# Optimization experiments

Hardware: AMD Instinct MI355X
Metric: run time of the kernel (lower is better)

Reference implementation:

```python
import jax, jax.numpy as jnp
import numpy as np

B = 2048
V = 50257
T = 64
D = 32
N_IN = 128
N_OUT = 128
N_HID = 1500
N_LAYERS = 5
N_BIAS = 2
K = 45  # int(edge_prob * n_nodes) fixed in-degree per receiving node
HID_PER_LAYER = N_HID // N_LAYERS  # 300
N_RECV = N_HID + N_OUT  # 1628 receiving nodes (hidden + output)


def _build_graph(rng):
    """Topological random wiring: each receiving node picks K predecessors
    among all earlier nodes (inputs, bias, earlier hidden layers)."""
    src_rows = []
    avail = N_IN + N_BIAS  # nodes available before first hidden layer
    for _ in range(N_LAYERS):
        src_rows.append(rng.integers(0, avail, size=(HID_PER_LAYER, K)))
        avail += HID_PER_LAYER
    src_rows.append(rng.integers(0, avail, size=(N_OUT, K)))  # output nodes
    return np.concatenate(src_rows, axis=0).astype(np.int32)  # [N_RECV, K]


def setup_inputs() -> dict:
    key = jax.random.key(0)
    ks = jax.random.split(key, 6)
    rng = np.random.default_rng(0)
    ids = jax.random.randint(ks[0], (B, T), 0, V, dtype=jnp.int32)
    token_emb = jax.random.normal(ks[1], (V, D), dtype=jnp.float32) * 0.02
    in_w = jax.random.normal(ks[2], (N_IN, T * D), dtype=jnp.float32) / np.sqrt(T * D)
    in_b = jnp.zeros((N_IN,), dtype=jnp.float32)
    src_idx = jnp.asarray(_build_graph(rng))  # [N_RECV, K] int32
    rwnn_w = jax.random.normal(ks[3], (N_RECV, K), dtype=jnp.float32) / np.sqrt(K)
    out_w = jax.random.normal(ks[4], (V, N_OUT), dtype=jnp.float32) / np.sqrt(N_OUT)
    out_b = jnp.zeros((V,), dtype=jnp.float32)
    return {"ids": ids, "token_emb": token_emb, "in_w": in_w, "in_b": in_b,
            "src_idx": src_idx, "rwnn_w": rwnn_w, "out_w": out_w, "out_b": out_b}


def _rwnn_forward(x, src_idx, rwnn_w):
    """x: [B, N_IN] -> [B, N_OUT]. Sparse random-wired DAG forward."""
    b = x.shape[0]
    vals = jnp.concatenate([x, jnp.ones((b, N_BIAS), dtype=x.dtype)], axis=1)
    off = 0
    for _ in range(N_LAYERS):
        s = src_idx[off:off + HID_PER_LAYER]          # [300, K]
        w = rwnn_w[off:off + HID_PER_LAYER]           # [300, K]
        gathered = vals[:, s]                          # [B, 300, K] irregular gather
        new = jnp.tanh(jnp.einsum('bnk,nk->bn', gathered, w))
        vals = jnp.concatenate([vals, new], axis=1)
        off += HID_PER_LAYER
    s = src_idx[off:off + N_OUT]
    w = rwnn_w[off:off + N_OUT]
    return jnp.tanh(jnp.einsum('bnk,nk->bn', vals[:, s], w))  # [B, N_OUT]


def reference(ids, token_emb, in_w, in_b, src_idx, rwnn_w, out_w, out_b):
    emb = token_emb[ids]                     # [B, T, D]
    flat = emb.reshape(emb.shape[0], T * D)  # [B, T*D]
    x = flat @ in_w.T + in_b                 # [B, N_IN]
    h = _rwnn_forward(x, src_idx, rwnn_w)    # [B, N_OUT]
    logits = h @ out_w.T + out_b             # [B, V]
    return logits
```

## Files before the change

kernel.cpp:

```cpp
#include <hip/hip_runtime.h>

#define B_SZ   2048
#define V_SZ   50257
#define TD     2048
#define NIN    128
#define NOUT   128
#define NRECV  1628
#define KDEG   45
#define KPAD   48
#define HPL    300
#define VALSN  1632

typedef __bf16 bf16x8 __attribute__((ext_vector_type(8)));
typedef float  floatx16 __attribute__((ext_vector_type(16)));

__device__ __forceinline__ unsigned short f2bf(float f) {
  unsigned u = __float_as_uint(f);
  u += 0x7fffu + ((u >> 16) & 1u);
  return (unsigned short)(u >> 16);
}

__device__ __forceinline__ float tanh_fast(float v) {
  float e = __builtin_amdgcn_exp2f(v * 2.88539008177793f);
  return 1.0f - 2.0f * __builtin_amdgcn_rcpf(1.0f + e);
}

__device__ __forceinline__ bf16x8 cvt8(float4 lo, float4 hi) {
  bf16x8 d;
  d[0] = (__bf16)lo.x; d[1] = (__bf16)lo.y; d[2] = (__bf16)lo.z; d[3] = (__bf16)lo.w;
  d[4] = (__bf16)hi.x; d[5] = (__bf16)hi.y; d[6] = (__bf16)hi.z; d[7] = (__bf16)hi.w;
  return d;
}

#define P1 1608224
#define P2 65536
#define P4 78144
#define PREP_TOTAL (P1 + P2 + P4)
#define PREP_BLOCKS ((PREP_TOTAL + 255) / 256)

__global__ __launch_bounds__(256) void prep_kernel(
    const float* __restrict__ in_w,
    const int* __restrict__ src, const float* __restrict__ rw,
    const float* __restrict__ out_w,
    unsigned short* __restrict__ inwb, unsigned short* __restrict__ outwb,
    int* __restrict__ iw) {
  int i = blockIdx.x * 256 + threadIdx.x;
  if (i < P1) {
    float4 v = ((const float4*)out_w)[i];
    ushort4 o; o.x = f2bf(v.x); o.y = f2bf(v.y); o.z = f2bf(v.z); o.w = f2bf(v.w);
    *(ushort4*)(outwb + (size_t)i * 4) = o;
    return;
  }
  i -= P1;
  if (i < P2) {
    float4 v = ((const float4*)in_w)[i];
    ushort4 o; o.x = f2bf(v.x); o.y = f2bf(v.y); o.z = f2bf(v.z); o.w = f2bf(v.w);
    *(ushort4*)(inwb + (size_t)i * 4) = o;
    return;
  }
  i -= P2;
  if (i < P4) {
    int r = i / KPAD, k = i - r * KPAD;
    int idx = 0; unsigned wb = 0;
    if (k < KDEG) {
      idx = src[r * KDEG + k];
      wb = __float_as_uint(rw[r * KDEG + k]);
    }
    iw[(size_t)i * 2] = idx;
    iw[(size_t)i * 2 + 1] = (int)wb;
  }
}

__global__ __launch_bounds__(256) void gemm1_kernel(
    const int* __restrict__ ids, const float* __restrict__ temb,
    const __bf16* __restrict__ inwb, const float* __restrict__ in_b,
    float* __restrict__ x) {
  int tid = threadIdx.x;
  int wv = tid >> 6, lane = tid & 63;
  int row = lane & 31, half = lane >> 5;
  int m0 = blockIdx.x * 32;
  int n0 = wv * 32;
  const int4* idq = (const int4*)(ids + (size_t)(m0 + row) * 64);
  const __bf16* bp = inwb + (size_t)(n0 + row) * TD + half * 8;
  floatx16 acc = (floatx16)0.0f;
  for (int t4 = 0; t4 < 16; ++t4) {
    int4 iq = idq[t4];
#pragma unroll
    for (int j = 0; j < 4; ++j) {
      int id = (j == 0) ? iq.x : (j == 1) ? iq.y : (j == 2) ? iq.z : iq.w;
      int t = t4 * 4 + j;
      const float* tp = temb + (size_t)id * 32;
      float4 a0 = *(const float4*)(tp + 8 * half);
      float4 a1 = *(const float4*)(tp + 8 * half + 4);
      float4 a2 = *(const float4*)(tp + 16 + 8 * half);
      float4 a3 = *(const float4*)(tp + 16 + 8 * half + 4);
      bf16x8 av0 = cvt8(a0, a1);
      bf16x8 av1 = cvt8(a2, a3);
      bf16x8 b0 = *(const bf16x8*)(bp + t * 32);
      bf16x8 b1 = *(const bf16x8*)(bp + t * 32 + 16);
      acc = __builtin_amdgcn_mfma_f32_32x32x16_bf16(av0, b0, acc, 0, 0, 0);
      acc = __builtin_amdgcn_mfma_f32_32x32x16_bf16(av1, b1, acc, 0, 0, 0);
    }
  }
  int col = n0 + row;
  float bias = in_b[col];
#pragma unroll
  for (int r = 0; r < 16; ++r) {
    int mrow = (r & 3) + 8 * (r >> 2) + 4 * half;
    x[(size_t)(m0 + mrow) * NIN + col] = acc[r] + bias;
  }
}

__global__ __launch_bounds__(512) void rwnn_kernel(
    const float* __restrict__ x, const int* __restrict__ iw,
    unsigned short* __restrict__ hb) {
  __shared__ float vals[VALSN * 8];
  int tid = threadIdx.x;
  int b0 = blockIdx.x * 8;
  {
    int p = tid & 7, n = tid >> 3;
    vals[n * 8 + p] = x[(b0 + p) * NIN + n];
    vals[(n + 64) * 8 + p] = x[(b0 + p) * NIN + n + 64];
    if (tid < 16) vals[(NIN + (tid >> 3)) * 8 + (tid & 7)] = 1.0f;
  }
  __syncthreads();
  int g = tid >> 2;
  int pq = (tid & 3) * 2;
  int base = NIN + 2;
  int off = 0;
  for (int layer = 0; layer < 5; ++layer) {
    for (int r = g; r < HPL; r += 128) {
      const int4* q4 = (const int4*)(iw) + (size_t)(off + r) * (KPAD / 2);
      float s0 = 0.f, s1 = 0.f;
#pragma unroll
      for (int k4 = 0; k4 < KPAD / 2; ++k4) {
        int4 q = q4[k4];
        float2 v0 = *(const float2*)(&vals[q.x * 8 + pq]);
        float w0 = __int_as_float(q.y);
        s0 += v0.x * w0; s1 += v0.y * w0;
        float2 v1 = *(const float2*)(&vals[q.z * 8 + pq]);
        float w1 = __int_as_float(q.w);
        s0 += v1.x * w1; s1 += v1.y * w1;
      }
      float2 o; o.x = tanh_fast(s0); o.y = tanh_fast(s1);
      *(float2*)(&vals[(base + r) * 8 + pq]) = o;
    }
    __syncthreads();
    off += HPL; base += HPL;
  }
  {
    int r = g;
    const int4* q4 = (const int4*)(iw) + (size_t)(off + r) * (KPAD / 2);
    float s0 = 0.f, s1 = 0.f;
#pragma unroll
    for (int k4 = 0; k4 < KPAD / 2; ++k4) {
      int4 q = q4[k4];
      float2 v0 = *(const float2*)(&vals[q.x * 8 + pq]);
      float w0 = __int_as_float(q.y);
      s0 += v0.x * w0; s1 += v0.y * w0;
      float2 v1 = *(const float2*)(&vals[q.z * 8 + pq]);
      float w1 = __int_as_float(q.w);
      s0 += v1.x * w1; s1 += v1.y * w1;
    }
    hb[(b0 + pq + 0) * NOUT + r] = f2bf(tanh_fast(s0));
    hb[(b0 + pq + 1) * NOUT + r] = f2bf(tanh_fast(s1));
  }
}

__global__ __launch_bounds__(256) void gemm3_kernel(
    const __bf16* __restrict__ h, const __bf16* __restrict__ wv,
    const float* __restrict__ out_b, float* __restrict__ out) {
  int tid = threadIdx.x;
  int wvid = tid >> 6, lane = tid & 63;
  int row = lane & 31, half = lane >> 5;
  int m0 = blockIdx.y * 128;
  int v0 = blockIdx.x * 128 + wvid * 32;
  int vr = v0 + row;
  int vc = vr < V_SZ ? vr : V_SZ - 1;
  const __bf16* bp = wv + (size_t)vc * NOUT + half * 8;
  bf16x8 bfrag[8];
#pragma unroll
  for (int s = 0; s < 8; ++s) bfrag[s] = *(const bf16x8*)(bp + s * 16);
  float bias = (vr < V_SZ) ? out_b[vr] : 0.f;
#pragma unroll
  for (int mt = 0; mt < 4; ++mt) {
    const __bf16* ap = h + (size_t)(m0 + mt * 32 + row) * NOUT + half * 8;
    floatx16 acc = (floatx16)0.0f;
#pragma unroll
    for (int s = 0; s < 8; ++s) {
      bf16x8 a = *(const bf16x8*)(ap + s * 16);
      acc = __builtin_amdgcn_mfma_f32_32x32x16_bf16(a, bfrag[s], acc, 0, 0, 0);
    }
    if (vr < V_SZ) {
#pragma unroll
      for (int r = 0; r < 16; ++r) {
        int mrow = (r & 3) + 8 * (r >> 2) + 4 * half;
        out[(size_t)(m0 + mt * 32 + mrow) * V_SZ + vr] = acc[r] + bias;
      }
    }
  }
}

extern "C" void kernel_launch(void* const* d_in, const int* in_sizes, int n_in,
                              void* d_out, int out_size, void* d_ws, size_t ws_size,
                              hipStream_t stream) {
  const int*   ids   = (const int*)d_in[0];
  const float* temb  = (const float*)d_in[1];
  const float* in_w  = (const float*)d_in[2];
  const float* in_b  = (const float*)d_in[3];
  const int*   src   = (const int*)d_in[4];
  const float* rw    = (const float*)d_in[5];
  const float* out_w = (const float*)d_in[6];
  const float* out_b = (const float*)d_in[7];
  float* out = (float*)d_out;

  char* ws = (char*)d_ws;
  unsigned short* inwb  = (unsigned short*)(ws + 8388608);
  unsigned short* outwb = (unsigned short*)(ws + 8912896);
  float*          x     = (float*)(ws + 21778688);
  unsigned short* hb    = (unsigned short*)(ws + 22827264);
  int*            iw    = (int*)(ws + 23351552);

  prep_kernel<<<PREP_BLOCKS, 256, 0, stream>>>(in_w, src, rw, out_w,
                                               inwb, outwb, iw);
  gemm1_kernel<<<64, 256, 0, stream>>>(ids, temb, (const __bf16*)inwb, in_b, x);
  rwnn_kernel<<<256, 512, 0, stream>>>(x, iw, hb);
  gemm3_kernel<<<dim3(393, 16), 256, 0, stream>>>((const __bf16*)hb,
                                                  (const __bf16*)outwb, out_b, out);
}
```

Baseline: 630.9 us.

## Halve RWNN batch per block and remap gemm3 tiles for XCD locality

The RWNN kernel now processes 4 batch rows per block instead of 8, with one sample per thread and twice as many blocks. This is meant to spread the sequential DAG work over more CUs and shrink shared memory per block, but it loads the index/weight stream twice as often per sample. Separately, the output GEMM remaps linear block IDs so that consecutive blocks on the same XCD (bid&7) work on contiguous tile ranges. The aim is better L2 reuse of the weight and activation tiles on MI355X's chiplet layout.

```diff
diff --git a/kernel.cpp b/kernel.cpp
--- a/kernel.cpp
+++ b/kernel.cpp
@@ -114,36 +114,30 @@
 __global__ __launch_bounds__(512) void rwnn_kernel(
     const float* __restrict__ x, const int* __restrict__ iw,
     unsigned short* __restrict__ hb) {
-  __shared__ float vals[VALSN * 8];
+  __shared__ float vals[VALSN * 4];
   int tid = threadIdx.x;
-  int b0 = blockIdx.x * 8;
+  int b0 = blockIdx.x * 4;
   {
-    int p = tid & 7, n = tid >> 3;
-    vals[n * 8 + p] = x[(b0 + p) * NIN + n];
-    vals[(n + 64) * 8 + p] = x[(b0 + p) * NIN + n + 64];
-    if (tid < 16) vals[(NIN + (tid >> 3)) * 8 + (tid & 7)] = 1.0f;
+    int p = tid & 3, n = tid >> 2;
+    vals[n * 4 + p] = x[(b0 + p) * NIN + n];
+    if (tid < 8) vals[(NIN + (tid >> 2)) * 4 + (tid & 3)] = 1.0f;
   }
   __syncthreads();
   int g = tid >> 2;
-  int pq = (tid & 3) * 2;
+  int pq = tid & 3;
   int base = NIN + 2;
   int off = 0;
   for (int layer = 0; layer < 5; ++layer) {
     for (int r = g; r < HPL; r += 128) {
       const int4* q4 = (const int4*)(iw) + (size_t)(off + r) * (KPAD / 2);
-      float s0 = 0.f, s1 = 0.f;
+      float s0 = 0.f;
 #pragma unroll
       for (int k4 = 0; k4 < KPAD / 2; ++k4) {
         int4 q = q4[k4];
-        float2 v0 = *(const float2*)(&vals[q.x * 8 + pq]);
-        float w0 = __int_as_float(q.y);
-        s0 += v0.x * w0; s1 += v0.y * w0;
-        float2 v1 = *(const float2*)(&vals[q.z * 8 + pq]);
-        float w1 = __int_as_float(q.w);
-        s0 += v1.x * w1; s1 += v1.y * w1;
+        s0 += vals[q.x * 4 + pq] * __int_as_float(q.y);
+        s0 += vals[q.z * 4 + pq] * __int_as_float(q.w);
       }
-      float2 o; o.x = tanh_fast(s0); o.y = tanh_fast(s1);
-      *(float2*)(&vals[(base + r) * 8 + pq]) = o;
+      vals[(base + r) * 4 + pq] = tanh_fast(s0);
     }
     __syncthreads();
     off += HPL; base += HPL;
@@ -151,19 +145,14 @@
   {
     int r = g;
     const int4* q4 = (const int4*)(iw) + (size_t)(off + r) * (KPAD / 2);
-    float s0 = 0.f, s1 = 0.f;
+    float s0 = 0.f;
 #pragma unroll
     for (int k4 = 0; k4 < KPAD / 2; ++k4) {
       int4 q = q4[k4];
-      float2 v0 = *(const float2*)(&vals[q.x * 8 + pq]);
-      float w0 = __int_as_float(q.y);
-      s0 += v0.x * w0; s1 += v0.y * w0;
-      float2 v1 = *(const float2*)(&vals[q.z * 8 + pq]);
-      float w1 = __int_as_float(q.w);
-      s0 += v1.x * w1; s1 += v1.y * w1;
-    }
-    hb[(b0 + pq + 0) * NOUT + r] = f2bf(tanh_fast(s0));
-    hb[(b0 + pq + 1) * NOUT + r] = f2bf(tanh_fast(s1));
+      s0 += vals[q.x * 4 + pq] * __int_as_float(q.y);
+      s0 += vals[q.z * 4 + pq] * __int_as_float(q.w);
+    }
+    hb[(b0 + pq) * NOUT + r] = f2bf(tanh_fast(s0));
   }
 }
 
@@ -173,8 +162,12 @@
   int tid = threadIdx.x;
   int wvid = tid >> 6, lane = tid & 63;
   int row = lane & 31, half = lane >> 5;
-  int m0 = blockIdx.y * 128;
-  int v0 = blockIdx.x * 128 + wvid * 32;
+  int bid = blockIdx.x + blockIdx.y * 393;
+  int L = (bid & 7) * 786 + (bid >> 3);
+  int mt = L / 393;
+  int vt = L - mt * 393;
+  int m0 = mt * 128;
+  int v0 = vt * 128 + wvid * 32;
   int vr = v0 + row;
   int vc = vr < V_SZ ? vr : V_SZ - 1;
   const __bf16* bp = wv + (size_t)vc * NOUT + half * 8;
@@ -183,8 +176,8 @@
   for (int s = 0; s < 8; ++s) bfrag[s] = *(const bf16x8*)(bp + s * 16);
   float bias = (vr < V_SZ) ? out_b[vr] : 0.f;
 #pragma unroll
-  for (int mt = 0; mt < 4; ++mt) {
-    const __bf16* ap = h + (size_t)(m0 + mt * 32 + row) * NOUT + half * 8;
+  for (int mtl = 0; mtl < 4; ++mtl) {
+    const __bf16* ap = h + (size_t)(m0 + mtl * 32 + row) * NOUT + half * 8;
     floatx16 acc = (floatx16)0.0f;
 #pragma unroll
     for (int s = 0; s < 8; ++s) {
@@ -195,7 +188,7 @@
 #pragma unroll
       for (int r = 0; r < 16; ++r) {
         int mrow = (r & 3) + 8 * (r >> 2) + 4 * half;
-        out[(size_t)(m0 + mt * 32 + mrow) * V_SZ + vr] = acc[r] + bias;
+        out[(size_t)(m0 + mtl * 32 + mrow) * V_SZ + vr] = acc[r] + bias;
       }
     }
   }
@@ -224,7 +217,7 @@
   prep_kernel<<<PREP_BLOCKS, 256, 0, stream>>>(in_w, src, rw, out_w,
                                                inwb, outwb, iw);
   gemm1_kernel<<<64, 256, 0, stream>>>(ids, temb, (const __bf16*)inwb, in_b, x);
-  rwnn_kernel<<<256, 512, 0, stream>>>(x, iw, hb);
+  rwnn_kernel<<<512, 512, 0, stream>>>(x, iw, hb);
   gemm3_kernel<<<dim3(393, 16), 256, 0, stream>>>((const __bf16*)hb,
                                                   (const __bf16*)outwb, out_b, out);
 }
```

Measured after the change: 644.8 us. 1.02x slower.
